# Performance work log

Hardware: AMD Instinct MI355X
Metric: run time of the kernel (lower is better)

## Reference

```python
import jax, jax.numpy as jnp
import numpy as np

D_MODEL, D_INNER, D_STATE, D_CONV, DT_RANK = 2048, 4096, 16, 4, 128
B, T = 2, 1024


def setup_inputs() -> dict:
    key = jax.random.key(0)
    ks = jax.random.split(key, 8)
    dt_init_std = DT_RANK ** -0.5
    # dt bias init per the torch code: inv softplus of dt in [dt_min, dt_max]
    dt = jnp.exp(jax.random.uniform(ks[6], (D_INNER,)) * (np.log(0.1) - np.log(0.001)) + np.log(0.001))
    dt = jnp.clip(dt, 1e-4, None)
    dt_proj_b = dt + jnp.log(-jnp.expm1(-dt))
    A_log = jnp.log(jnp.tile(jnp.arange(1, D_STATE + 1, dtype=jnp.float32)[None, :], (D_INNER, 1)))
    return {
        "x": jax.random.normal(ks[0], (B, T, D_MODEL), jnp.float32),
        "h": jnp.zeros((B, D_INNER, D_STATE), jnp.float32),
        "conv_cache": jnp.zeros((B, D_INNER, D_CONV - 1), jnp.float32),
        "in_proj_w": jax.random.normal(ks[1], (2 * D_INNER, D_MODEL), jnp.float32) * 0.02,
        "conv_w": jax.random.normal(ks[2], (D_INNER, D_CONV), jnp.float32) * (1.0 / np.sqrt(D_CONV)),
        "conv_b": jnp.zeros((D_INNER,), jnp.float32),
        "x_proj_w": jax.random.normal(ks[3], (DT_RANK + 2 * D_STATE, D_INNER), jnp.float32) * 0.02,
        "dt_proj_w": jax.random.uniform(ks[4], (D_INNER, DT_RANK), jnp.float32, -dt_init_std, dt_init_std),
        "dt_proj_b": dt_proj_b,
        "A_log": A_log,
        "D_param": jnp.ones((D_INNER,), jnp.float32),
        "out_proj_w": jax.random.normal(ks[5], (D_MODEL, D_INNER), jnp.float32) * 0.02,
    }


def _forward(x, h, conv_cache, in_proj_w, conv_w, conv_b, x_proj_w,
             dt_proj_w, dt_proj_b, A_log, D_param, out_proj_w):
    Tlen = x.shape[1]
    xz = x @ in_proj_w.T                                  # (B,T,2*d_inner)
    xi, z = jnp.split(xz, 2, axis=-1)
    # causal depthwise conv with cache: concat history then valid conv
    xc = jnp.concatenate([jnp.swapaxes(conv_cache, 1, 2), xi], axis=1)  # (B,T+3,d_inner)
    new_conv_cache = jnp.swapaxes(xc[:, -(D_CONV - 1):, :], 1, 2)       # (B,d_inner,3)
    xconv = sum(xc[:, k:k + Tlen, :] * conv_w[:, k] for k in range(D_CONV)) + conv_b
    xs = jax.nn.silu(xconv)                               # (B,T,d_inner)
    # SSM params per step
    dbc = xs @ x_proj_w.T                                 # (B,T,dt_rank+2n)
    delta, Bm, Cm = jnp.split(dbc, [DT_RANK, DT_RANK + D_STATE], axis=-1)
    delta = jax.nn.softplus(delta @ dt_proj_w.T + dt_proj_b)  # (B,T,d_inner)
    A = -jnp.exp(A_log)                                   # (d_inner,n)
    dA = jnp.exp(jnp.einsum('btd,dn->btdn', delta, A))    # (B,T,d,n)
    dBx = jnp.einsum('btd,btn,btd->btdn', delta, Bm, xs)  # (B,T,d,n)

    def step(hc, inp):
        dA_t, dBx_t, C_t = inp
        hc = dA_t * hc + dBx_t                            # (B,d,n)
        return hc, jnp.einsum('bdn,bn->bd', hc, C_t)

    h_last, ys = jax.lax.scan(
        step, h,
        (jnp.moveaxis(dA, 1, 0), jnp.moveaxis(dBx, 1, 0), jnp.moveaxis(Cm, 1, 0)))
    y = jnp.moveaxis(ys, 0, 1) + D_param * xs             # (B,T,d_inner)
    out = (y * jax.nn.silu(z)) @ out_proj_w.T             # (B,T,d_model)
    return out, h_last, new_conv_cache


def reference(x, h, conv_cache, in_proj_w, conv_w, conv_b, x_proj_w,
              dt_proj_w, dt_proj_b, A_log, D_param, out_proj_w):
    return _forward(x, h, conv_cache, in_proj_w, conv_w, conv_b, x_proj_w,
                    dt_proj_w, dt_proj_b, A_log, D_param, out_proj_w)
```

## Files before the change

kernel.cpp:

```cpp
#include <hip/hip_runtime.h>
#include <hip/hip_bf16.h>
#include <math.h>

#define D_MODEL 2048
#define D_INNER 4096
#define D_STATE 16
#define D_CONV  4
#define DT_RANK 128
#define NB      2
#define TT      1024
#define M_TOT   (NB * TT)
#define NC      16
#define CL      64
#define TC      16

typedef __bf16 bf16x8_t __attribute__((ext_vector_type(8)));
typedef float  f32x4_t  __attribute__((ext_vector_type(4)));

__global__ __launch_bounds__(256) void fused_cast(
    const float* __restrict__ x,  const float* __restrict__ wi,
    const float* __restrict__ wo, const float* __restrict__ wx,
    const float* __restrict__ wdt,
    __bf16* __restrict__ x16,  __bf16* __restrict__ wi16,
    __bf16* __restrict__ wo16, __bf16* __restrict__ wx16,
    __bf16* __restrict__ wdt16, __bf16* __restrict__ dbc16,
    __bf16* __restrict__ out16)
{
    const size_t g = (size_t)blockIdx.x * 256 + threadIdx.x;
    const float* src; __bf16* dst; size_t off;
    if      (g < 524288)  { src = x;   dst = x16;   off = g; }
    else if (g < 2621440) { src = wi;  dst = wi16;  off = g - 524288; }
    else if (g < 3670016) { src = wo;  dst = wo16;  off = g - 2621440; }
    else if (g < 3801088) { off = g - 3670016; dst = wx16;
                            src = (g < 3751936) ? wx : nullptr; }
    else if (g < 3866624) { src = wdt; dst = wdt16; off = g - 3801088; }
    else if (g < 3948544) { src = nullptr; dst = dbc16; off = g - 3866624; }
    else                  { src = nullptr; dst = out16; off = g - 3948544; }

    bf16x8_t v;
    if (src) {
        const float4 f0 = ((const float4*)src)[2 * off];
        const float4 f1 = ((const float4*)src)[2 * off + 1];
        v[0] = (__bf16)f0.x; v[1] = (__bf16)f0.y; v[2] = (__bf16)f0.z; v[3] = (__bf16)f0.w;
        v[4] = (__bf16)f1.x; v[5] = (__bf16)f1.y; v[6] = (__bf16)f1.z; v[7] = (__bf16)f1.w;
    } else {
        v = (bf16x8_t)(__bf16)0.f;
    }
    ((bf16x8_t*)dst)[off] = v;
}

template <int EPI, int KSTEP, typename OutT>
__global__ __launch_bounds__(256) void gemm_bf16_nt(
    const __bf16* __restrict__ A, int lda,
    const __bf16* __restrict__ W, int ldw,
    OutT* __restrict__ C, int ldc,
    int Kloop, int Nmax, const float* __restrict__ bias)
{
    __shared__ __bf16 As[128 * KSTEP];
    __shared__ __bf16 Bs[128 * KSTEP];

    const int tid  = threadIdx.x;
    const int wave = tid >> 6;
    const int lane = tid & 63;
    const int m0 = blockIdx.y * 128;
    const int n0 = blockIdx.x * 128;
    const int mw = (wave >> 1) * 64;
    const int nw = (wave & 1) * 64;
    const int koff = blockIdx.z * Kloop;

    f32x4_t acc[4][4] = {};

    const int g0 = wave * 2;
    const int rA = g0 * 16 + (lane >> 2);
    const int kk = (lane & 3) * 8;

    const __bf16* gA0 = A + (size_t)(m0 + rA) * lda + kk + koff;
    const __bf16* gA1 = gA0 + (size_t)16 * lda;
    const __bf16* gB0 = W + (size_t)(n0 + rA) * ldw + kk + koff;
    const __bf16* gB1 = gB0 + (size_t)16 * ldw;

    __bf16* lA0 = &As[(size_t)g0 * 512];
    __bf16* lA1 = &As[(size_t)(g0 + 1) * 512];
    __bf16* lB0 = &Bs[(size_t)g0 * 512];
    __bf16* lB1 = &Bs[(size_t)(g0 + 1) * 512];

    const int fr = lane & 15;
    const int fk = (lane >> 4) * 8;

    for (int k0 = 0; k0 < Kloop; k0 += KSTEP) {
#pragma unroll
        for (int p = 0; p < KSTEP / 32; p++) {
            const int kp = k0 + p * 32;
            const int lp = p * 4096;
            __builtin_amdgcn_global_load_lds(
                (const __attribute__((address_space(1))) void*)(gA0 + kp),
                (__attribute__((address_space(3))) void*)(lA0 + lp), 16, 0, 0);
            __builtin_amdgcn_global_load_lds(
                (const __attribute__((address_space(1))) void*)(gA1 + kp),
                (__attribute__((address_space(3))) void*)(lA1 + lp), 16, 0, 0);
            __builtin_amdgcn_global_load_lds(
                (const __attribute__((address_space(1))) void*)(gB0 + kp),
                (__attribute__((address_space(3))) void*)(lB0 + lp), 16, 0, 0);
            __builtin_amdgcn_global_load_lds(
                (const __attribute__((address_space(1))) void*)(gB1 + kp),
                (__attribute__((address_space(3))) void*)(lB1 + lp), 16, 0, 0);
        }
        __syncthreads();

#pragma unroll
        for (int p = 0; p < KSTEP / 32; p++) {
            const int lp = p * 4096;
            bf16x8_t av[4], bv[4];
#pragma unroll
            for (int mt = 0; mt < 4; mt++)
                av[mt] = *(const bf16x8_t*)&As[lp + (mw + mt * 16 + fr) * 32 + fk];
#pragma unroll
            for (int nt = 0; nt < 4; nt++)
                bv[nt] = *(const bf16x8_t*)&Bs[lp + (nw + nt * 16 + fr) * 32 + fk];

#pragma unroll
            for (int mt = 0; mt < 4; mt++)
#pragma unroll
                for (int nt = 0; nt < 4; nt++)
                    acc[mt][nt] = __builtin_amdgcn_mfma_f32_16x16x32_bf16(
                        av[mt], bv[nt], acc[mt][nt], 0, 0, 0);
        }
        __syncthreads();
    }

    const int cn = n0 + nw + (lane & 15);
    const int rb = m0 + mw + (lane >> 4) * 4;
#pragma unroll
    for (int mt = 0; mt < 4; mt++)
#pragma unroll
        for (int nt = 0; nt < 4; nt++) {
            const int n = cn + nt * 16;
            if (n >= Nmax) continue;
#pragma unroll
            for (int r = 0; r < 4; r++) {
                float v = acc[mt][nt][r];
                OutT* p = &C[(size_t)(rb + mt * 16 + r) * ldc + n];
                if (EPI == 1) {
                    v += bias[n];
                    v = (v > 20.f) ? v : log1pf(__expf(v));
                    *p = (OutT)v;
                } else if (EPI == 2) {
                    atomicAdd((float*)p, v);
                } else {
                    *p = (OutT)v;
                }
            }
        }
}

__global__ __launch_bounds__(256) void gemm_dt(
    const float* __restrict__ A,
    const __bf16* __restrict__ W,
    __bf16* __restrict__ C,
    const float* __restrict__ bias)
{
    __shared__ __bf16 As[4 * 64 * 32];
    __shared__ __bf16 Bs[4 * 64 * 32];

    const int tid  = threadIdx.x;
    const int wave = tid >> 6;
    const int lane = tid & 63;
    const int m0 = blockIdx.y * 64;
    const int n0 = blockIdx.x * 64;
    const int mw = (wave >> 1) * 32;
    const int nw = (wave & 1) * 32;

    {
        const int r  = tid >> 2;
        const int cg = (tid & 3) * 8;
        const float* gA = A + (size_t)(m0 + r) * 160 + cg;
#pragma unroll
        for (int p = 0; p < 4; p++) {
            const float4 f0 = *(const float4*)(gA + p * 32);
            const float4 f1 = *(const float4*)(gA + p * 32 + 4);
            bf16x8_t v;
            v[0] = (__bf16)f0.x; v[1] = (__bf16)f0.y; v[2] = (__bf16)f0.z; v[3] = (__bf16)f0.w;
            v[4] = (__bf16)f1.x; v[5] = (__bf16)f1.y; v[6] = (__bf16)f1.z; v[7] = (__bf16)f1.w;
            *(bf16x8_t*)&As[p * 2048 + r * 32 + cg] = v;
        }
    }
    {
        const int rB = wave * 16 + (lane >> 2);
        const int kk = (lane & 3) * 8;
        const __bf16* gB = W + (size_t)(n0 + rB) * 128 + kk;
        __bf16* lB = &Bs[wave * 512];
#pragma unroll
        for (int p = 0; p < 4; p++) {
            __builtin_amdgcn_global_load_lds(
                (const __attribute__((address_space(1))) void*)(gB + p * 32),
                (__attribute__((address_space(3))) void*)(lB + p * 2048), 16, 0, 0);
        }
    }
    __syncthreads();

    const int fr = lane & 15;
    const int fk = (lane >> 4) * 8;
    f32x4_t acc[2][2] = {};
#pragma unroll
    for (int p = 0; p < 4; p++) {
        bf16x8_t av[2], bv[2];
#pragma unroll
        for (int mt = 0; mt < 2; mt++)
            av[mt] = *(const bf16x8_t*)&As[p * 2048 + (mw + mt * 16 + fr) * 32 + fk];
#pragma unroll
        for (int nt = 0; nt < 2; nt++)
            bv[nt] = *(const bf16x8_t*)&Bs[p * 2048 + (nw + nt * 16 + fr) * 32 + fk];
#pragma unroll
        for (int mt = 0; mt < 2; mt++)
#pragma unroll
            for (int nt = 0; nt < 2; nt++)
                acc[mt][nt] = __builtin_amdgcn_mfma_f32_16x16x32_bf16(
                    av[mt], bv[nt], acc[mt][nt], 0, 0, 0);
    }

    const int cn = n0 + nw + (lane & 15);
    const int rb = m0 + mw + (lane >> 4) * 4;
#pragma unroll
    for (int mt = 0; mt < 2; mt++)
#pragma unroll
        for (int nt = 0; nt < 2; nt++) {
            const int n = cn + nt * 16;
            const float bs = bias[n];
#pragma unroll
            for (int r = 0; r < 4; r++) {
                float v = acc[mt][nt][r] + bs;
                v = (v > 20.f) ? v : log1pf(__expf(v));
                C[(size_t)(rb + mt * 16 + r) * 4096 + n] = (__bf16)v;
            }
        }
}

__global__ __launch_bounds__(256) void conv_silu(
    const __bf16* __restrict__ xz16,
    const float* __restrict__ conv_cache,
    const float* __restrict__ conv_w,
    const float* __restrict__ conv_b,
    __bf16* __restrict__ xs16,
    float* __restrict__ cc_out)
{
    const int b  = blockIdx.z;
    const int d  = blockIdx.y * 256 + threadIdx.x;
    const int t0 = blockIdx.x * TC;

    const float4 w  = *(const float4*)&conv_w[d * 4];
    const float bias = conv_b[d];

    float v[TC + 3];
    if (t0 == 0) {
        v[0] = conv_cache[(b * D_INNER + d) * 3 + 0];
        v[1] = conv_cache[(b * D_INNER + d) * 3 + 1];
        v[2] = conv_cache[(b * D_INNER + d) * 3 + 2];
    } else {
        v[0] = (float)xz16[(size_t)(b * TT + t0 - 3) * 8192 + d];
        v[1] = (float)xz16[(size_t)(b * TT + t0 - 2) * 8192 + d];
        v[2] = (float)xz16[(size_t)(b * TT + t0 - 1) * 8192 + d];
    }
#pragma unroll
    for (int k = 0; k < TC; k++)
        v[k + 3] = (float)xz16[(size_t)(b * TT + t0 + k) * 8192 + d];

#pragma unroll
    for (int k = 0; k < TC; k++) {
        float c = v[k] * w.x + v[k + 1] * w.y + v[k + 2] * w.z + v[k + 3] * w.w + bias;
        float s = c / (1.f + __expf(-c));
        xs16[(size_t)(b * TT + t0 + k) * 4096 + d] = (__bf16)s;
    }

    if (t0 + TC == TT) {
        cc_out[(b * D_INNER + d) * 3 + 0] = v[TC];
        cc_out[(b * D_INNER + d) * 3 + 1] = v[TC + 1];
        cc_out[(b * D_INNER + d) * 3 + 2] = v[TC + 2];
    }
}

__global__ __launch_bounds__(256) void scan_phase_a(
    const __bf16* __restrict__ delta16,
    const float* __restrict__ dbc,
    const __bf16* __restrict__ xs16,
    const float* __restrict__ A_log,
    float* __restrict__ P,
    float* __restrict__ S)
{
    const int idx = blockIdx.x * 256 + threadIdx.x;
    const int sub = idx & 3;
    const int d   = (idx >> 2) & 4095;
    const int c   = (idx >> 14) & (NC - 1);
    const int b   = idx >> 18;

    const float4 Af = *(const float4*)&A_log[d * 16 + sub * 4];
    const float Ad0 = -__expf(Af.x), Ad1 = -__expf(Af.y);
    const float Ad2 = -__expf(Af.z), Ad3 = -__expf(Af.w);

    const int t0 = c * CL;
    const __bf16* pdelta = delta16 + (size_t)(b * TT + t0) * 4096 + d;
    const __bf16* px     = xs16 + (size_t)(b * TT + t0) * 4096 + d;
    const float*  pB     = dbc + ((size_t)b * TT + t0) * 160 + 128 + sub * 4;

    float h0 = 0.f, h1 = 0.f, h2 = 0.f, h3 = 0.f, sd = 0.f;
#pragma unroll 4
    for (int t = 0; t < CL; t++) {
        const float delta = (float)pdelta[(size_t)t * 4096];
        const float xv    = (float)px[(size_t)t * 4096];
        const float4 Bv   = *(const float4*)&pB[(size_t)t * 160];
        const float dx = delta * xv;
        h0 = __expf(delta * Ad0) * h0 + dx * Bv.x;
        h1 = __expf(delta * Ad1) * h1 + dx * Bv.y;
        h2 = __expf(delta * Ad2) * h2 + dx * Bv.z;
        h3 = __expf(delta * Ad3) * h3 + dx * Bv.w;
        sd += delta;
    }
    const size_t o = ((size_t)(b * NC + c) * 4096 + d) * 16 + sub * 4;
    *(float4*)&P[o] = make_float4(__expf(Ad0 * sd), __expf(Ad1 * sd),
                                  __expf(Ad2 * sd), __expf(Ad3 * sd));
    *(float4*)&S[o] = make_float4(h0, h1, h2, h3);
}

__global__ __launch_bounds__(256) void scan_phase_c(
    const __bf16* __restrict__ delta16,
    const __bf16* __restrict__ xz16,
    const float* __restrict__ dbc,
    const __bf16* __restrict__ xs16,
    const float* __restrict__ P,
    const float* __restrict__ S,
    const float* __restrict__ h_in,
    const float* __restrict__ A_log,
    const float* __restrict__ D_param,
    __bf16* __restrict__ ys16,
    float* __restrict__ h_out)
{
    const int idx = blockIdx.x * 256 + threadIdx.x;
    const int sub = idx & 3;
    const int d   = (idx >> 2) & 4095;
    const int c   = (idx >> 14) & (NC - 1);
    const int b   = idx >> 18;

    const float4 Af = *(const float4*)&A_log[d * 16 + sub * 4];
    const float Ad0 = -__expf(Af.x), Ad1 = -__expf(Af.y);
    const float Ad2 = -__expf(Af.z), Ad3 = -__expf(Af.w);
    const float Dp = D_param[d];

    float4 hf = *(const float4*)&h_in[((size_t)b * 4096 + d) * 16 + sub * 4];
    float h0 = hf.x, h1 = hf.y, h2 = hf.z, h3 = hf.w;
    for (int cc = 0; cc < c; cc++) {
        const size_t o2 = ((size_t)(b * NC + cc) * 4096 + d) * 16 + sub * 4;
        const float4 p = *(const float4*)&P[o2];
        const float4 s = *(const float4*)&S[o2];
        h0 = p.x * h0 + s.x;
        h1 = p.y * h1 + s.y;
        h2 = p.z * h2 + s.z;
        h3 = p.w * h3 + s.w;
    }

    const int t0 = c * CL;
    const __bf16* pdelta = delta16 + (size_t)(b * TT + t0) * 4096 + d;
    const __bf16* pz     = xz16 + (size_t)(b * TT + t0) * 8192 + 4096 + d;
    const __bf16* px     = xs16 + (size_t)(b * TT + t0) * 4096 + d;
    const float*  pB     = dbc + ((size_t)b * TT + t0) * 160 + 128 + sub * 4;
    const float*  pC     = pB + 16;
    __bf16* py = ys16 + (size_t)(b * TT + t0) * 4096 + d;

#pragma unroll 4
    for (int t = 0; t < CL; t++) {
        const float delta = (float)pdelta[(size_t)t * 4096];
        const float xv    = (float)px[(size_t)t * 4096];
        const float4 Bv   = *(const float4*)&pB[(size_t)t * 160];
        const float4 Cv   = *(const float4*)&pC[(size_t)t * 160];
        const float dx = delta * xv;

        h0 = __expf(delta * Ad0) * h0 + dx * Bv.x;
        h1 = __expf(delta * Ad1) * h1 + dx * Bv.y;
        h2 = __expf(delta * Ad2) * h2 + dx * Bv.z;
        h3 = __expf(delta * Ad3) * h3 + dx * Bv.w;

        float y = h0 * Cv.x + h1 * Cv.y + h2 * Cv.z + h3 * Cv.w;
        y += __shfl_xor(y, 1);
        y += __shfl_xor(y, 2);

        if (sub == 0) {
            const float zv = (float)pz[(size_t)t * 8192];
            y += Dp * xv;
            const float g = zv / (1.f + __expf(-zv));
            py[(size_t)t * 4096] = (__bf16)(y * g);
        }
    }

    if (c == NC - 1) {
        *(float4*)&h_out[((size_t)b * 4096 + d) * 16 + sub * 4] =
            make_float4(h0, h1, h2, h3);
    }
}

extern "C" void kernel_launch(void* const* d_in, const int* in_sizes, int n_in,
                              void* d_out, int out_size, void* d_ws, size_t ws_size,
                              hipStream_t stream)
{
    const float* x          = (const float*)d_in[0];
    const float* h_in       = (const float*)d_in[1];
    const float* conv_cache = (const float*)d_in[2];
    const float* in_proj_w  = (const float*)d_in[3];
    const float* conv_w     = (const float*)d_in[4];
    const float* conv_b     = (const float*)d_in[5];
    const float* x_proj_w   = (const float*)d_in[6];
    const float* dt_proj_w  = (const float*)d_in[7];
    const float* dt_proj_b  = (const float*)d_in[8];
    const float* A_log      = (const float*)d_in[9];
    const float* D_param    = (const float*)d_in[10];
    const float* out_proj_w = (const float*)d_in[11];

    float* out    = (float*)d_out;
    float* h_out  = (float*)d_out + (size_t)NB * TT * D_MODEL;
    float* cc_out = h_out + (size_t)NB * D_INNER * D_STATE;

    char* ws = (char*)d_ws;
    __bf16* xz16    = (__bf16*)(ws);
    __bf16* x16     = (__bf16*)(ws + 33554432);
    float*  Pbuf    = (float*)(ws + 33554432);
    __bf16* wi16    = (__bf16*)(ws + 41943040);
    __bf16* delta16 = (__bf16*)(ws + 41943040);
    float*  Sbuf    = (float*)(ws + 58720256);
    __bf16* wo16    = (__bf16*)(ws + 75497472);
    __bf16* xs16    = (__bf16*)(ws + 92274688);
    float*  dbc     = (float*)(ws + 109051904);
    __bf16* ys16    = (__bf16*)(ws + 110362624);
    __bf16* wx16    = (__bf16*)(ws + 127139840);
    __bf16* wdt16   = (__bf16*)(ws + 129236992);

    dim3 blk(256);

    fused_cast<<<dim3(19520), blk, 0, stream>>>(
        x, in_proj_w, out_proj_w, x_proj_w, dt_proj_w,
        x16, wi16, wo16, wx16, wdt16, (__bf16*)dbc, (__bf16*)out);

    gemm_bf16_nt<0, 64, __bf16><<<dim3(64, 16, 1), blk, 0, stream>>>(
        x16, 2048, wi16, 2048, xz16, 8192, 2048, 8192, nullptr);

    conv_silu<<<dim3(TT / TC, D_INNER / 256, NB), blk, 0, stream>>>(
        xz16, conv_cache, conv_w, conv_b, xs16, cc_out);

    gemm_bf16_nt<2, 32, float><<<dim3(2, 16, 16), blk, 0, stream>>>(
        xs16, 4096, wx16, 4096, dbc, 160, 256, 160, nullptr);

    gemm_dt<<<dim3(64, 32), blk, 0, stream>>>(dbc, wdt16, delta16, dt_proj_b);

    scan_phase_a<<<dim3(NB * D_INNER * NC * 4 / 256), blk, 0, stream>>>(
        delta16, dbc, xs16, A_log, Pbuf, Sbuf);
    scan_phase_c<<<dim3(NB * D_INNER * NC * 4 / 256), blk, 0, stream>>>(
        delta16, xz16, dbc, xs16, Pbuf, Sbuf, h_in, A_log, D_param, ys16, h_out);

    gemm_bf16_nt<2, 64, float><<<dim3(16, 16, 2), blk, 0, stream>>>(
        ys16, 4096, wo16, 4096, out, 2048, 2048, 2048, nullptr);
}
```

Measured before the change: 475.9 us.

## Add 256x256-tile in_proj GEMM with direct global-to-LDS multi-stage loads

Replaces the 128x128 in_proj GEMM with a new 512-thread kernel using 256x256 tiles and K-step 32. It loads tiles straight into LDS with global_load_lds across a four-slot ring, keeps two K-steps in flight, swizzles LDS addresses, and raises wave priority around MFMA bursts. The goal is more data reuse per tile and better overlap of memory loads with matrix math. In exchange it uses many more accumulator registers per thread and launches fewer blocks (256), which may limit occupancy or leave CUs idle.

```diff
diff --git a/kernel.cpp b/kernel.cpp
--- a/kernel.cpp
+++ b/kernel.cpp
@@ -47,6 +47,117 @@
         v = (bf16x8_t)(__bf16)0.f;
     }
     ((bf16x8_t*)dst)[off] = v;
+}
+
+__global__ __launch_bounds__(512, 2) void gemm_bf16_256(
+    const __bf16* __restrict__ A, int lda,
+    const __bf16* __restrict__ W, int ldw,
+    __bf16* __restrict__ C, int ldc,
+    int nt)
+{
+    __shared__ __bf16 As[4 * 256 * 32];
+    __shared__ __bf16 Bs[4 * 256 * 32];
+
+    const int tid = threadIdx.x;
+    const int w   = tid >> 6;
+    const int l   = tid & 63;
+    const int m0  = blockIdx.y * 256;
+    const int n0  = blockIdx.x * 256;
+    const int wm  = (w >> 2) * 128;
+    const int wn  = (w & 3) * 64;
+
+    const int ml   = ((l >> 2) ^ (l >> 4)) & 3;
+    const int scol = ((l & 3) ^ ml) * 8;
+    const int srow = w * 16 + (l >> 2);
+    const __bf16* gA = A + (size_t)(m0 + srow) * lda + scol;
+    const __bf16* gB = W + (size_t)(n0 + srow) * ldw + scol;
+    __bf16* lA = &As[(size_t)(w * 16) * 32];
+    __bf16* lB = &Bs[(size_t)(w * 16) * 32];
+
+    const int fr = l & 15;
+    const int sw = (((l >> 4) ^ (fr & 3) ^ ((fr >> 2) & 3)) & 3) * 8;
+    const int aoff = (wm + fr) * 32 + sw;
+    const int boff = (wn + fr) * 32 + sw;
+
+    f32x4_t acc[8][4] = {};
+
+#define STAGE_A(t, q) { \
+    const __bf16* s0_ = gA + (size_t)(t) * 32; \
+    __builtin_amdgcn_global_load_lds((const __attribute__((address_space(1))) void*)s0_, \
+        (__attribute__((address_space(3))) void*)(lA + (q) * 8192), 16, 0, 0); \
+    __builtin_amdgcn_global_load_lds((const __attribute__((address_space(1))) void*)(s0_ + (size_t)128 * lda), \
+        (__attribute__((address_space(3))) void*)(lA + (q) * 8192 + 128 * 32), 16, 0, 0); }
+#define STAGE_B(t, q) { \
+    const __bf16* s0_ = gB + (size_t)(t) * 32; \
+    __builtin_amdgcn_global_load_lds((const __attribute__((address_space(1))) void*)s0_, \
+        (__attribute__((address_space(3))) void*)(lB + (q) * 8192), 16, 0, 0); \
+    __builtin_amdgcn_global_load_lds((const __attribute__((address_space(1))) void*)(s0_ + (size_t)128 * ldw), \
+        (__attribute__((address_space(3))) void*)(lB + (q) * 8192 + 128 * 32), 16, 0, 0); }
+
+    STAGE_A(0, 0); STAGE_B(0, 0);
+    STAGE_A(1, 1); STAGE_B(1, 1);
+    asm volatile("s_waitcnt vmcnt(4)" ::: "memory");
+    __builtin_amdgcn_s_barrier();
+
+    for (int t = 0; t < nt; ++t) {
+        const int q  = t & 3;
+        const int qn = (t + 2) & 3;
+        const __bf16* Aq = &As[q * 8192];
+        const __bf16* Bq = &Bs[q * 8192];
+        bf16x8_t av[4], bv[4];
+
+#pragma unroll
+        for (int i = 0; i < 4; i++)
+            av[i] = *(const bf16x8_t*)&Aq[aoff + i * 512];
+#pragma unroll
+        for (int i = 0; i < 4; i++)
+            bv[i] = *(const bf16x8_t*)&Bq[boff + i * 512];
+        if (t + 2 < nt) STAGE_A(t + 2, qn);
+        __builtin_amdgcn_s_barrier();
+        asm volatile("s_waitcnt lgkmcnt(0)" ::: "memory");
+        __builtin_amdgcn_sched_barrier(0);
+        __builtin_amdgcn_s_setprio(1);
+#pragma unroll
+        for (int mt = 0; mt < 4; mt++)
+#pragma unroll
+            for (int nn = 0; nn < 4; nn++)
+                acc[mt][nn] = __builtin_amdgcn_mfma_f32_16x16x32_bf16(
+                    av[mt], bv[nn], acc[mt][nn], 0, 0, 0);
+        __builtin_amdgcn_s_setprio(0);
+        __builtin_amdgcn_s_barrier();
+
+#pragma unroll
+        for (int i = 0; i < 4; i++)
+            av[i] = *(const bf16x8_t*)&Aq[aoff + (i + 4) * 512];
+        if (t + 2 < nt) STAGE_B(t + 2, qn);
+        __builtin_amdgcn_s_barrier();
+        asm volatile("s_waitcnt lgkmcnt(0)" ::: "memory");
+        __builtin_amdgcn_sched_barrier(0);
+        __builtin_amdgcn_s_setprio(1);
+#pragma unroll
+        for (int mt = 0; mt < 4; mt++)
+#pragma unroll
+            for (int nn = 0; nn < 4; nn++)
+                acc[mt + 4][nn] = __builtin_amdgcn_mfma_f32_16x16x32_bf16(
+                    av[mt], bv[nn], acc[mt + 4][nn], 0, 0, 0);
+        __builtin_amdgcn_s_setprio(0);
+        if (t + 2 < nt) asm volatile("s_waitcnt vmcnt(4)" ::: "memory");
+        else            asm volatile("s_waitcnt vmcnt(0)" ::: "memory");
+        __builtin_amdgcn_s_barrier();
+    }
+#undef STAGE_A
+#undef STAGE_B
+
+    const int cn = n0 + wn + fr;
+    const int rb = m0 + wm + (l >> 4) * 4;
+#pragma unroll
+    for (int mt = 0; mt < 8; mt++)
+#pragma unroll
+        for (int nn = 0; nn < 4; nn++)
+#pragma unroll
+            for (int r = 0; r < 4; r++)
+                C[(size_t)(rb + mt * 16 + r) * ldc + cn + nn * 16] =
+                    (__bf16)acc[mt][nn][r];
 }
 
 template <int EPI, int KSTEP, typename OutT>
@@ -436,8 +547,8 @@
         x, in_proj_w, out_proj_w, x_proj_w, dt_proj_w,
         x16, wi16, wo16, wx16, wdt16, (__bf16*)dbc, (__bf16*)out);
 
-    gemm_bf16_nt<0, 64, __bf16><<<dim3(64, 16, 1), blk, 0, stream>>>(
-        x16, 2048, wi16, 2048, xz16, 8192, 2048, 8192, nullptr);
+    gemm_bf16_256<<<dim3(32, 8), dim3(512), 0, stream>>>(
+        x16, 2048, wi16, 2048, xz16, 8192, 2048 / 32);
 
     conv_silu<<<dim3(TT / TC, D_INNER / 256, NB), blk, 0, stream>>>(
         xz16, conv_cache, conv_w, conv_b, xs16, cc_out);
```

New measurement: 459.6 us. -3.4%, faster.
